# Kernel tuning notes

Measured on AMD Instinct MI355X. Metric: run time of the kernel, lower is better.

Reference implementation:

```python
import jax, jax.numpy as jnp
import numpy as np

N_NODES = 100_000
N_EDGES = 1_600_000
N_GRAPHS = 1_000
NODES_PER_GRAPH = 100
N_NODE_FEATS = 64
DIM_STATE = 32
DIM_OUT = 64
DIM_NODE_EMB = 64
HID = 128
HEADS = 8
BASES = 4


def _lin(key, out_f, in_f, bias=True):
    k1, k2 = jax.random.split(key)
    lim = 1.0 / np.sqrt(in_f)
    w = jax.random.uniform(k1, (out_f, in_f), minval=-lim, maxval=lim, dtype=jnp.float32)
    if not bias:
        return w
    b = jax.random.uniform(k2, (out_f,), minval=-lim, maxval=lim, dtype=jnp.float32)
    return w, b


def setup_inputs() -> dict:
    key = jax.random.key(0)
    ks = jax.random.split(key, 16)
    x = jax.random.normal(ks[0], (N_NODES, N_NODE_FEATS), dtype=jnp.float32)
    edge_index = jax.random.randint(ks[1], (2, N_EDGES), 0, N_NODES, dtype=jnp.int32)
    batch = jnp.arange(N_NODES, dtype=jnp.int32) // NODES_PER_GRAPH  # sorted segment ids
    n_atoms = jnp.full((N_GRAPHS, 1), NODES_PER_GRAPH, dtype=jnp.int32)  # consistent with batch
    z_e = jax.random.normal(ks[2], (N_GRAPHS, DIM_STATE), dtype=jnp.float32)
    nfc_w, nfc_b = _lin(ks[3], HID, N_NODE_FEATS)
    # EGConv: bases Linear(in, (out//heads)*bases, no bias); comb Linear(in, heads*bases); bias (out,)
    gc1_bases_w = _lin(ks[4], (HID // HEADS) * BASES, HID, bias=False)
    gc1_comb_w, gc1_comb_b = _lin(ks[5], HEADS * BASES, HID)
    gc1_bias = jnp.zeros((HID,), jnp.float32)
    gc2_bases_w = _lin(ks[6], (DIM_NODE_EMB // HEADS) * BASES, HID, bias=False)
    gc2_comb_w, gc2_comb_b = _lin(ks[7], HEADS * BASES, HID)
    gc2_bias = jnp.zeros((DIM_NODE_EMB,), jnp.float32)
    attn_w, attn_b = _lin(ks[8], 1, DIM_NODE_EMB + DIM_STATE)
    fcg_w, fcg_b = _lin(ks[9], DIM_OUT, DIM_NODE_EMB)
    fccg_w, fccg_b = _lin(ks[10], DIM_OUT, DIM_NODE_EMB)
    return {"x": x, "edge_index": edge_index, "batch": batch, "n_atoms": n_atoms, "z_e": z_e,
            "nfc_w": nfc_w, "nfc_b": nfc_b,
            "gc1_bases_w": gc1_bases_w, "gc1_comb_w": gc1_comb_w, "gc1_comb_b": gc1_comb_b, "gc1_bias": gc1_bias,
            "gc2_bases_w": gc2_bases_w, "gc2_comb_w": gc2_comb_w, "gc2_comb_b": gc2_comb_b, "gc2_bias": gc2_bias,
            "attn_w": attn_w, "attn_b": attn_b, "fcg_w": fcg_w, "fcg_b": fcg_b, "fccg_w": fccg_w, "fccg_b": fccg_b}


def _egconv(h, src, dst, bases_w, comb_w, comb_b, bias, heads=HEADS, nbases=BASES):
    # PyG EGConv with aggregators=['symnorm'], add_self_loops=True
    n = h.shape[0]
    out_ch = bias.shape[0]
    deg = jnp.ones((n,), h.dtype).at[dst].add(1.0)          # in-degree + self loop
    dis = jax.lax.rsqrt(deg)                                 # deg^-1/2
    b = h @ bases_w.T                                        # [n, nbases*(out_ch//heads)]
    # symnorm aggregation incl. self-loop term dis_i^2 * b_i
    agg = ((dis * dis)[:, None] * b).at[dst].add((dis[src] * dis[dst])[:, None] * b[src])
    w = (h @ comb_w.T + comb_b).reshape(n, heads, nbases)    # [n, H, B]
    agg = agg.reshape(n, nbases, out_ch // heads)            # [n, B, F/H]
    return jnp.einsum('nhb,nbf->nhf', w, agg).reshape(n, out_ch) + bias


def reference(x, edge_index, batch, n_atoms, z_e, nfc_w, nfc_b,
              gc1_bases_w, gc1_comb_w, gc1_comb_b, gc1_bias,
              gc2_bases_w, gc2_comb_w, gc2_comb_b, gc2_bias,
              attn_w, attn_b, fcg_w, fcg_b, fccg_w, fccg_b):
    src, dst = edge_index[0], edge_index[1]
    h = jax.nn.elu(x @ nfc_w.T + nfc_b)
    h = jax.nn.elu(_egconv(h, src, dst, gc1_bases_w, gc1_comb_w, gc1_comb_b, gc1_bias))
    h = jax.nn.elu(_egconv(h, src, dst, gc2_bases_w, gc2_comb_w, gc2_comb_b, gc2_bias))
    h = h / jnp.maximum(jnp.linalg.norm(h, axis=1, keepdims=True), 1e-12)  # L2 normalize
    z_a = jax.ops.segment_sum(h, batch, num_segments=N_GRAPHS) @ fcg_w.T + fcg_b
    z_rep = jnp.repeat(z_e, n_atoms[:, 0], axis=0, total_repeat_length=N_NODES)
    logits = jnp.concatenate([h, z_rep], axis=1) @ attn_w.T + attn_b + 1e-16  # [N,1]
    m = jax.ops.segment_max(logits, batch, num_segments=N_GRAPHS)
    e = jnp.exp(logits - m[batch])
    denom = jax.ops.segment_sum(e, batch, num_segments=N_GRAPHS) + 1e-16
    attns = e / denom[batch]
    z_c = jax.ops.segment_sum(attns * h, batch, num_segments=N_GRAPHS) @ fccg_w.T + fccg_b
    return z_a, z_c, h
```

## Files before the change

kernel.cpp:

```cpp
#include <hip/hip_runtime.h>
#include <hip/hip_bf16.h>
#include <math.h>

#define N_NODES  100000
#define N_EDGES  1600000
#define N_GRAPHS 1000
#define NPG      100
#define NBKT     391
#define EPB      4096

typedef float  f32x4 __attribute__((ext_vector_type(4)));
typedef short  s16x8 __attribute__((ext_vector_type(8)));

__device__ __forceinline__ float elu_f(float x) {
    return x > 0.0f ? x : expm1f(x);
}
__device__ __forceinline__ float bf2f(unsigned int u16) {
    union { unsigned int i; float f; } v; v.i = u16 << 16; return v.f;
}
__device__ __forceinline__ unsigned short f2bf(float f) {
    __hip_bfloat16 h = __float2bfloat16(f);
    return *reinterpret_cast<unsigned short*>(&h);
}
__device__ __forceinline__ s16x8 cvt8(const float4& a, const float4& b) {
    s16x8 o;
    o[0]=(short)f2bf(a.x); o[1]=(short)f2bf(a.y); o[2]=(short)f2bf(a.z); o[3]=(short)f2bf(a.w);
    o[4]=(short)f2bf(b.x); o[5]=(short)f2bf(b.y); o[6]=(short)f2bf(b.z); o[7]=(short)f2bf(b.w);
    return o;
}

__global__ __launch_bounds__(512) void zero_bkt_k(int* __restrict__ bkt_cnt) {
    int t = threadIdx.x;
    if (t < NBKT) bkt_cnt[t] = 0;
}

__global__ __launch_bounds__(256) void bincount_k(const int* __restrict__ ei, int* __restrict__ bkt_cnt) {
    __shared__ int h[NBKT];
    const int t = threadIdx.x;
    for (int i = t; i < NBKT; i += 256) h[i] = 0;
    __syncthreads();
    const int4* dst4 = (const int4*)(ei + N_EDGES);
    int i0 = blockIdx.x * (EPB / 4);
    for (int i = t; i < EPB / 4; i += 256) {
        int g = i0 + i;
        if (g < N_EDGES / 4) {
            int4 d = dst4[g];
            atomicAdd(&h[d.x >> 8], 1);
            atomicAdd(&h[d.y >> 8], 1);
            atomicAdd(&h[d.z >> 8], 1);
            atomicAdd(&h[d.w >> 8], 1);
        }
    }
    __syncthreads();
    for (int i = t; i < NBKT; i += 256)
        if (h[i]) atomicAdd(&bkt_cnt[i], h[i]);
}

__global__ __launch_bounds__(512) void bkt_scan_k(const int* __restrict__ bkt_cnt,
                                                  int* __restrict__ bkt_start,
                                                  int* __restrict__ bkt_cursor)
{
    __shared__ int s[512];
    int t = threadIdx.x;
    s[t] = (t < NBKT) ? bkt_cnt[t] : 0;
    __syncthreads();
    #pragma unroll
    for (int off = 1; off < 512; off <<= 1) {
        int u = (t >= off) ? s[t - off] : 0;
        __syncthreads();
        s[t] += u;
        __syncthreads();
    }
    if (t <= NBKT) {
        int v = (t == 0) ? 0 : s[t - 1];
        bkt_start[t] = v;
        if (t < NBKT) bkt_cursor[t] = v;
    }
}

__global__ __launch_bounds__(256) void binscatter_k(const int* __restrict__ ei,
                                                    int* __restrict__ bkt_cursor,
                                                    int2* __restrict__ pairs)
{
    __shared__ int h[NBKT];
    __shared__ int base[NBKT];
    const int t = threadIdx.x;
    for (int i = t; i < NBKT; i += 256) h[i] = 0;
    __syncthreads();
    const int4* src4 = (const int4*)ei;
    const int4* dst4 = (const int4*)(ei + N_EDGES);
    int i0 = blockIdx.x * (EPB / 4);
    for (int i = t; i < EPB / 4; i += 256) {
        int g = i0 + i;
        if (g < N_EDGES / 4) {
            int4 d = dst4[g];
            atomicAdd(&h[d.x >> 8], 1);
            atomicAdd(&h[d.y >> 8], 1);
            atomicAdd(&h[d.z >> 8], 1);
            atomicAdd(&h[d.w >> 8], 1);
        }
    }
    __syncthreads();
    for (int i = t; i < NBKT; i += 256) {
        int c = h[i];
        base[i] = c ? atomicAdd(&bkt_cursor[i], c) : 0;
        h[i] = 0;
    }
    __syncthreads();
    for (int i = t; i < EPB / 4; i += 256) {
        int g = i0 + i;
        if (g < N_EDGES / 4) {
            int4 s4 = src4[g];
            int4 d4 = dst4[g];
            int b, r;
            b = d4.x >> 8; r = atomicAdd(&h[b], 1); pairs[base[b] + r] = make_int2(s4.x, d4.x);
            b = d4.y >> 8; r = atomicAdd(&h[b], 1); pairs[base[b] + r] = make_int2(s4.y, d4.y);
            b = d4.z >> 8; r = atomicAdd(&h[b], 1); pairs[base[b] + r] = make_int2(s4.z, d4.z);
            b = d4.w >> 8; r = atomicAdd(&h[b], 1); pairs[base[b] + r] = make_int2(s4.w, d4.w);
        }
    }
}

__global__ __launch_bounds__(256) void bucket_csr_k(const int2* __restrict__ pairs,
                                                    const int* __restrict__ bkt_start,
                                                    int* __restrict__ starts,
                                                    int* __restrict__ cnt,
                                                    float* __restrict__ dis,
                                                    int* __restrict__ srclist)
{
    __shared__ int s[256];
    __shared__ int cur[256];
    const int b = blockIdx.x, t = threadIdx.x;
    const int lo = bkt_start[b], hi = bkt_start[b + 1];
    const int n0 = b << 8;
    const int nn = min(256, N_NODES - n0);

    s[t] = 0;
    __syncthreads();
    for (int i = lo + t; i < hi; i += 256) {
        int2 p = pairs[i];
        atomicAdd(&s[p.y & 255], 1);
    }
    __syncthreads();
    int v = s[t];
    __syncthreads();
    s[t] = v;
    __syncthreads();
    #pragma unroll
    for (int off = 1; off < 256; off <<= 1) {
        int u = (t >= off) ? s[t - off] : 0;
        __syncthreads();
        s[t] += u;
        __syncthreads();
    }
    int ex = lo + s[t] - v;
    if (t < nn) {
        starts[n0 + t] = ex;
        cnt[n0 + t] = v;
        dis[n0 + t] = rsqrtf(1.0f + (float)v);
    }
    cur[t] = ex;
    __syncthreads();
    for (int i = lo + t; i < hi; i += 256) {
        int2 p = pairs[i];
        int pos = atomicAdd(&cur[p.y & 255], 1);
        srclist[pos] = p.x;
    }
}

template<int K, int N1, int N2, int WR, int WC, int RT, int CT, bool AF32>
__global__ __launch_bounds__(256) void mgemm_k(
    const void* __restrict__ Av, const float* __restrict__ W1,
    const float* __restrict__ W2, const float* __restrict__ bias,
    const float* __restrict__ dis,
    void* __restrict__ out1, float* __restrict__ out2, int M)
{
    constexpr int KT = K / 32;
    const int t = threadIdx.x;
    const int wave = t >> 6, lane = t & 63;
    const int wr = wave / WC, wc = wave % WC;
    const int lr = lane & 15, lk = lane >> 4;
    const int blockRow = blockIdx.x * (WR * RT * 16);

    f32x4 acc[RT][CT];
    #pragma unroll
    for (int rt = 0; rt < RT; ++rt)
        #pragma unroll
        for (int ct = 0; ct < CT; ++ct)
            acc[rt][ct] = (f32x4){0.f, 0.f, 0.f, 0.f};

    const float*          Af = (const float*)Av;
    const unsigned short* Ab = (const unsigned short*)Av;

    #pragma unroll
    for (int kt = 0; kt < KT; ++kt) {
        const int k0 = kt * 32 + lk * 8;
        s16x8 afr[RT];
        #pragma unroll
        for (int rt = 0; rt < RT; ++rt) {
            int r = blockRow + (wr * RT + rt) * 16 + lr;
            r = (r < M) ? r : (M - 1);
            if constexpr (AF32) {
                const float* ap = Af + (size_t)r * K + k0;
                float4 v1 = *(const float4*)ap;
                float4 v2 = *(const float4*)(ap + 4);
                afr[rt] = cvt8(v1, v2);
            } else {
                afr[rt] = *(const s16x8*)(Ab + (size_t)r * K + k0);
            }
        }
        s16x8 bfr[CT];
        #pragma unroll
        for (int ct = 0; ct < CT; ++ct) {
            int n = (wc * CT + ct) * 16 + lr;
            const float* wp = (N2 == 0 || n < N1) ? (W1 + (size_t)n * K + k0)
                                                  : (W2 + (size_t)(n - N1) * K + k0);
            float4 v1 = *(const float4*)wp;
            float4 v2 = *(const float4*)(wp + 4);
            bfr[ct] = cvt8(v1, v2);
        }
        #pragma unroll
        for (int rt = 0; rt < RT; ++rt)
            #pragma unroll
            for (int ct = 0; ct < CT; ++ct)
                acc[rt][ct] = __builtin_amdgcn_mfma_f32_16x16x32_bf16(afr[rt], bfr[ct], acc[rt][ct], 0, 0, 0);
    }

    #pragma unroll
    for (int rt = 0; rt < RT; ++rt) {
        int mbase = blockRow + (wr * RT + rt) * 16 + lk * 4;
        #pragma unroll
        for (int j = 0; j < 4; ++j) {
            int m = mbase + j;
            if (m >= M) continue;
            float dsc = (N2 == 0) ? 1.0f : dis[m];
            #pragma unroll
            for (int ct = 0; ct < CT; ++ct) {
                int n = (wc * CT + ct) * 16 + lr;
                float v = acc[rt][ct][j];
                if constexpr (N2 == 0) {
                    v = elu_f(v + bias[n]);
                    ((unsigned short*)out1)[(size_t)m * N1 + n] = f2bf(v);
                } else {
                    if (n < N1) {
                        ((unsigned short*)out1)[(size_t)m * N1 + n] = f2bf(dsc * v);
                    } else {
                        out2[(size_t)m * N2 + (n - N1)] = v + bias[n - N1];
                    }
                }
            }
        }
    }
}

__global__ __launch_bounds__(256) void gather1_k(
    const int* __restrict__ starts, const int* __restrict__ cnt,
    const int* __restrict__ srclist, const unsigned short* __restrict__ c,
    const float* __restrict__ w1, const float* __restrict__ dis,
    const float* __restrict__ bias, unsigned short* __restrict__ h2b)
{
    __shared__ float aggS[4][68];

    const int t = threadIdx.x;
    const int nn   = t >> 6;
    const int lane = t & 63;
    const int q    = lane & 15;
    const int slot = lane >> 4;
    const int n    = blockIdx.x * 4 + nn;

    const int s0 = starts[n];
    const int cn = cnt[n];
    float a0 = 0.f, a1 = 0.f, a2 = 0.f, a3 = 0.f;
    if (slot == 0) {
        uint2 u = *(const uint2*)(c + (size_t)n * 64 + q * 4);
        a0 = bf2f(u.x & 0xffff); a1 = bf2f(u.x >> 16);
        a2 = bf2f(u.y & 0xffff); a3 = bf2f(u.y >> 16);
    }
    for (int j = slot; j < cn; j += 4) {
        int src = srclist[s0 + j];
        uint2 u = *(const uint2*)(c + (size_t)src * 64 + q * 4);
        a0 += bf2f(u.x & 0xffff); a1 += bf2f(u.x >> 16);
        a2 += bf2f(u.y & 0xffff); a3 += bf2f(u.y >> 16);
    }
    a0 += __shfl_xor(a0, 16, 64); a0 += __shfl_xor(a0, 32, 64);
    a1 += __shfl_xor(a1, 16, 64); a1 += __shfl_xor(a1, 32, 64);
    a2 += __shfl_xor(a2, 16, 64); a2 += __shfl_xor(a2, 32, 64);
    a3 += __shfl_xor(a3, 16, 64); a3 += __shfl_xor(a3, 32, 64);
    if (slot == 0) {
        aggS[nn][q * 4 + 0] = a0;
        aggS[nn][q * 4 + 1] = a1;
        aggS[nn][q * 4 + 2] = a2;
        aggS[nn][q * 4 + 3] = a3;
    }
    __syncthreads();

    const float dn = dis[n];
    const float* wr = w1 + (size_t)n * 32;
    unsigned short* out = h2b + (size_t)n * 128;
    #pragma unroll
    for (int r = 0; r < 2; ++r) {
        int j = r * 64 + lane;
        int hh = j >> 4, f = j & 15;
        float4 wv = *(const float4*)(wr + hh * 4);
        float s = wv.x * aggS[nn][0 * 16 + f] + wv.y * aggS[nn][1 * 16 + f]
                + wv.z * aggS[nn][2 * 16 + f] + wv.w * aggS[nn][3 * 16 + f];
        float v = elu_f(s * dn + bias[j]);
        out[j] = f2bf(v);
    }
}

__global__ __launch_bounds__(256) void gather2_k(
    const int* __restrict__ starts, const int* __restrict__ cnt,
    const int* __restrict__ srclist, const unsigned short* __restrict__ c,
    const float* __restrict__ w2, const float* __restrict__ dis,
    const float* __restrict__ bias, float* __restrict__ hout)
{
    __shared__ float aggS[4][36];

    const int t = threadIdx.x;
    const int nn   = t >> 6;
    const int lane = t & 63;
    const int q    = lane & 15;
    const int slot = lane >> 4;
    const int n    = blockIdx.x * 4 + nn;

    const int s0 = starts[n];
    const int cn = cnt[n];
    float a0 = 0.f, a1 = 0.f;
    if (slot == 0) {
        unsigned int u = *(const unsigned int*)(c + (size_t)n * 32 + q * 2);
        a0 = bf2f(u & 0xffff); a1 = bf2f(u >> 16);
    }
    for (int j = slot; j < cn; j += 4) {
        int src = srclist[s0 + j];
        unsigned int u = *(const unsigned int*)(c + (size_t)src * 32 + q * 2);
        a0 += bf2f(u & 0xffff); a1 += bf2f(u >> 16);
    }
    a0 += __shfl_xor(a0, 16, 64); a0 += __shfl_xor(a0, 32, 64);
    a1 += __shfl_xor(a1, 16, 64); a1 += __shfl_xor(a1, 32, 64);
    if (slot == 0) {
        aggS[nn][q * 2 + 0] = a0;
        aggS[nn][q * 2 + 1] = a1;
    }
    __syncthreads();

    const float dn = dis[n];
    const int hh = lane >> 3, f = lane & 7;
    float4 wv = *(const float4*)(w2 + (size_t)n * 32 + hh * 4);
    float s = wv.x * aggS[nn][0 * 8 + f] + wv.y * aggS[nn][1 * 8 + f]
            + wv.z * aggS[nn][2 * 8 + f] + wv.w * aggS[nn][3 * 8 + f];
    float sv = elu_f(s * dn + bias[lane]);

    float tot = sv * sv;
    #pragma unroll
    for (int o = 1; o < 64; o <<= 1) tot += __shfl_xor(tot, o, 64);
    float inv = 1.0f / fmaxf(sqrtf(tot), 1e-12f);
    hout[(size_t)n * 64 + lane] = sv * inv;
}

__global__ __launch_bounds__(128) void graph_k(const float* __restrict__ h,
                                               const float* __restrict__ z_e,
                                               const float* __restrict__ aw,
                                               const float* __restrict__ ab,
                                               const float* __restrict__ fcgw,
                                               const float* __restrict__ fcgb,
                                               const float* __restrict__ fccgw,
                                               const float* __restrict__ fccgb,
                                               float* __restrict__ z_a,
                                               float* __restrict__ z_c)
{
    __shared__ float Hs[NPG * 64];
    __shared__ float sumh[64], wsh[64], lg[NPG], ex[NPG];
    __shared__ float red[2];
    int g = blockIdx.x, t = threadIdx.x;
    const float* hg = h + (size_t)g * NPG * 64;
    for (int idx = t; idx < NPG * 64; idx += 128) Hs[idx] = hg[idx];
    __syncthreads();

    if (t < 64) {
        float s = 0.0f;
        for (int n = 0; n < NPG; ++n) s += Hs[n * 64 + t];
        sumh[t] = s;
    }
    __syncthreads();

    if (t < 64) {
        float acc = fcgb[t];
        for (int f = 0; f < 64; ++f) acc = fmaf(sumh[f], fcgw[t * 64 + f], acc);
        z_a[(size_t)g * 64 + t] = acc;
    }
    if (t < NPG) {
        float zd = 0.0f;
        for (int q = 0; q < 32; ++q) zd = fmaf(z_e[(size_t)g * 32 + q], aw[64 + q], zd);
        float dot = 0.0f;
        for (int k0 = 0; k0 < 64; ++k0) {
            int k = (k0 + t) & 63;
            dot = fmaf(Hs[t * 64 + k], aw[k], dot);
        }
        lg[t] = dot + zd + ab[0] + 1e-16f;
    }
    __syncthreads();

    if (t < 64) {
        float m = -INFINITY;
        for (int n = t; n < NPG; n += 64) m = fmaxf(m, lg[n]);
        #pragma unroll
        for (int o = 1; o < 64; o <<= 1) m = fmaxf(m, __shfl_xor(m, o, 64));
        if (t == 0) red[0] = m;
    }
    __syncthreads();
    float m = red[0];
    if (t < NPG) ex[t] = expf(lg[t] - m);
    __syncthreads();
    if (t < 64) {
        float s = 0.0f;
        for (int n = t; n < NPG; n += 64) s += ex[n];
        #pragma unroll
        for (int o = 1; o < 64; o <<= 1) s += __shfl_xor(s, o, 64);
        if (t == 0) red[1] = s + 1e-16f;
    }
    __syncthreads();
    float inv_denom = 1.0f / red[1];
    if (t < 64) {
        float a = 0.0f;
        for (int n = 0; n < NPG; ++n) a = fmaf(ex[n], Hs[n * 64 + t], a);
        wsh[t] = a * inv_denom;
    }
    __syncthreads();
    if (t < 64) {
        float acc = fccgb[t];
        for (int f = 0; f < 64; ++f) acc = fmaf(wsh[f], fccgw[t * 64 + f], acc);
        z_c[(size_t)g * 64 + t] = acc;
    }
}

extern "C" void kernel_launch(void* const* d_in, const int* in_sizes, int n_in,
                              void* d_out, int out_size, void* d_ws, size_t ws_size,
                              hipStream_t stream)
{
    const float* x     = (const float*)d_in[0];
    const int*   ei    = (const int*)d_in[1];
    const float* z_e   = (const float*)d_in[4];
    const float* nfc_w = (const float*)d_in[5];
    const float* nfc_b = (const float*)d_in[6];
    const float* g1bw  = (const float*)d_in[7];
    const float* g1cw  = (const float*)d_in[8];
    const float* g1cb  = (const float*)d_in[9];
    const float* g1b   = (const float*)d_in[10];
    const float* g2bw  = (const float*)d_in[11];
    const float* g2cw  = (const float*)d_in[12];
    const float* g2cb  = (const float*)d_in[13];
    const float* g2b   = (const float*)d_in[14];
    const float* aw    = (const float*)d_in[15];
    const float* ab    = (const float*)d_in[16];
    const float* fcgw  = (const float*)d_in[17];
    const float* fcgb  = (const float*)d_in[18];
    const float* fccgw = (const float*)d_in[19];
    const float* fccgb = (const float*)d_in[20];

    float* ws        = (float*)d_ws;
    float* dis       = ws;
    int*   cnt       = (int*)(ws + 102400);
    int*   starts    = cnt + 102400;
    int*   bkt_cnt   = starts + 102400;
    int*   bkt_start = bkt_cnt + 512;
    int*   bkt_cur   = bkt_start + 512;
    int*   srclist   = bkt_cur + 512;
    float* hbuf      = (float*)(srclist + 1600000);
    float* c1f       = hbuf + 6400000;
    float* w1        = c1f + 3200000;
    float* w2        = w1 + 3200000;
    unsigned short* hb = (unsigned short*)hbuf;
    unsigned short* c1 = (unsigned short*)c1f;
    unsigned short* c2 = (unsigned short*)c1f;
    int2*  pairs     = (int2*)hbuf;

    float* z_a  = (float*)d_out;
    float* z_c  = z_a + (size_t)N_GRAPHS * 64;
    float* hout = z_a + (size_t)2 * N_GRAPHS * 64;

    const int GB = (N_NODES + 63) / 64;

    zero_bkt_k<<<1, 512, 0, stream>>>(bkt_cnt);
    bincount_k<<<(N_EDGES + EPB - 1) / EPB, 256, 0, stream>>>(ei, bkt_cnt);
    bkt_scan_k<<<1, 512, 0, stream>>>(bkt_cnt, bkt_start, bkt_cur);
    binscatter_k<<<(N_EDGES + EPB - 1) / EPB, 256, 0, stream>>>(ei, bkt_cur, pairs);
    bucket_csr_k<<<NBKT, 256, 0, stream>>>(pairs, bkt_start, starts, cnt, dis, srclist);

    mgemm_k<64, 128, 0, 2, 2, 2, 4, true>
        <<<GB, 256, 0, stream>>>(x, nfc_w, nullptr, nfc_b, dis, hb, nullptr, N_NODES);
    mgemm_k<128, 64, 32, 2, 2, 2, 3, false>
        <<<GB, 256, 0, stream>>>(hb, g1bw, g1cw, g1cb, dis, c1, w1, N_NODES);
    gather1_k<<<N_NODES / 4, 256, 0, stream>>>(starts, cnt, srclist, c1, w1, dis, g1b, hb);
    mgemm_k<128, 32, 32, 2, 2, 2, 2, false>
        <<<GB, 256, 0, stream>>>(hb, g2bw, g2cw, g2cb, dis, c2, w2, N_NODES);
    gather2_k<<<N_NODES / 4, 256, 0, stream>>>(starts, cnt, srclist, c2, w2, dis, g2b, hout);
    graph_k<<<N_GRAPHS, 128, 0, stream>>>(hout, z_e, aw, ab, fcgw, fcgb, fccgw, fccgb, z_a, z_c);
}
```

Measured before the change: 294.1 us.

## Fuse node-feature GEMM with gc1 projection and gather1 with gc2 projection

```diff
diff --git a/kernel.cpp b/kernel.cpp
--- a/kernel.cpp
+++ b/kernel.cpp
@@ -168,144 +168,195 @@
     }
 }
 
-template<int K, int N1, int N2, int WR, int WC, int RT, int CT, bool AF32>
-__global__ __launch_bounds__(256) void mgemm_k(
-    const void* __restrict__ Av, const float* __restrict__ W1,
-    const float* __restrict__ W2, const float* __restrict__ bias,
-    const float* __restrict__ dis,
-    void* __restrict__ out1, float* __restrict__ out2, int M)
-{
-    constexpr int KT = K / 32;
+__global__ __launch_bounds__(256) void fusedA_k(
+    const float* __restrict__ x, const float* __restrict__ W0, const float* __restrict__ b0,
+    const float* __restrict__ Wc, const float* __restrict__ Ww, const float* __restrict__ bw,
+    const float* __restrict__ dis, unsigned short* __restrict__ c1out,
+    float* __restrict__ w1out, int M)
+{
+    __shared__ unsigned short hT[64][136];
     const int t = threadIdx.x;
     const int wave = t >> 6, lane = t & 63;
-    const int wr = wave / WC, wc = wave % WC;
     const int lr = lane & 15, lk = lane >> 4;
-    const int blockRow = blockIdx.x * (WR * RT * 16);
-
-    f32x4 acc[RT][CT];
-    #pragma unroll
-    for (int rt = 0; rt < RT; ++rt)
-        #pragma unroll
-        for (int ct = 0; ct < CT; ++ct)
-            acc[rt][ct] = (f32x4){0.f, 0.f, 0.f, 0.f};
-
-    const float*          Af = (const float*)Av;
-    const unsigned short* Ab = (const unsigned short*)Av;
-
-    #pragma unroll
-    for (int kt = 0; kt < KT; ++kt) {
-        const int k0 = kt * 32 + lk * 8;
-        s16x8 afr[RT];
-        #pragma unroll
-        for (int rt = 0; rt < RT; ++rt) {
-            int r = blockRow + (wr * RT + rt) * 16 + lr;
-            r = (r < M) ? r : (M - 1);
-            if constexpr (AF32) {
-                const float* ap = Af + (size_t)r * K + k0;
-                float4 v1 = *(const float4*)ap;
-                float4 v2 = *(const float4*)(ap + 4);
-                afr[rt] = cvt8(v1, v2);
-            } else {
-                afr[rt] = *(const s16x8*)(Ab + (size_t)r * K + k0);
-            }
-        }
-        s16x8 bfr[CT];
-        #pragma unroll
-        for (int ct = 0; ct < CT; ++ct) {
-            int n = (wc * CT + ct) * 16 + lr;
-            const float* wp = (N2 == 0 || n < N1) ? (W1 + (size_t)n * K + k0)
-                                                  : (W2 + (size_t)(n - N1) * K + k0);
-            float4 v1 = *(const float4*)wp;
-            float4 v2 = *(const float4*)(wp + 4);
-            bfr[ct] = cvt8(v1, v2);
-        }
-        #pragma unroll
-        for (int rt = 0; rt < RT; ++rt)
-            #pragma unroll
-            for (int ct = 0; ct < CT; ++ct)
-                acc[rt][ct] = __builtin_amdgcn_mfma_f32_16x16x32_bf16(afr[rt], bfr[ct], acc[rt][ct], 0, 0, 0);
-    }
-
-    #pragma unroll
-    for (int rt = 0; rt < RT; ++rt) {
-        int mbase = blockRow + (wr * RT + rt) * 16 + lk * 4;
+    const int blockRow = blockIdx.x * 64;
+
+    {
+        const int wr = wave >> 1, wc = wave & 1;
+        f32x4 acc[2][4];
+        #pragma unroll
+        for (int rt = 0; rt < 2; ++rt)
+            #pragma unroll
+            for (int ct = 0; ct < 4; ++ct) acc[rt][ct] = (f32x4){0.f,0.f,0.f,0.f};
+
+        #pragma unroll
+        for (int kt = 0; kt < 2; ++kt) {
+            const int k0 = kt * 32 + lk * 8;
+            s16x8 afr[2];
+            #pragma unroll
+            for (int rt = 0; rt < 2; ++rt) {
+                int r = blockRow + (wr * 2 + rt) * 16 + lr;
+                r = (r < M) ? r : (M - 1);
+                const float* ap = x + (size_t)r * 64 + k0;
+                afr[rt] = cvt8(*(const float4*)ap, *(const float4*)(ap + 4));
+            }
+            s16x8 bfr[4];
+            #pragma unroll
+            for (int ct = 0; ct < 4; ++ct) {
+                int n = (wc * 4 + ct) * 16 + lr;
+                const float* wp = W0 + (size_t)n * 64 + k0;
+                bfr[ct] = cvt8(*(const float4*)wp, *(const float4*)(wp + 4));
+            }
+            #pragma unroll
+            for (int rt = 0; rt < 2; ++rt)
+                #pragma unroll
+                for (int ct = 0; ct < 4; ++ct)
+                    acc[rt][ct] = __builtin_amdgcn_mfma_f32_16x16x32_bf16(afr[rt], bfr[ct], acc[rt][ct], 0, 0, 0);
+        }
+        #pragma unroll
+        for (int rt = 0; rt < 2; ++rt) {
+            int lmb = (wr * 2 + rt) * 16 + lk * 4;
+            #pragma unroll
+            for (int j = 0; j < 4; ++j) {
+                #pragma unroll
+                for (int ct = 0; ct < 4; ++ct) {
+                    int n = (wc * 4 + ct) * 16 + lr;
+                    float v = elu_f(acc[rt][ct][j] + b0[n]);
+                    hT[lmb + j][n] = f2bf(v);
+                }
+            }
+        }
+    }
+    __syncthreads();
+
+    {
+        f32x4 acc[6];
+        #pragma unroll
+        for (int ct = 0; ct < 6; ++ct) acc[ct] = (f32x4){0.f,0.f,0.f,0.f};
+        #pragma unroll
+        for (int kt = 0; kt < 4; ++kt) {
+            const int k0 = kt * 32 + lk * 8;
+            s16x8 af = *(const s16x8*)&hT[wave * 16 + lr][k0];
+            #pragma unroll
+            for (int ct = 0; ct < 6; ++ct) {
+                int n = ct * 16 + lr;
+                const float* wp = (n < 64) ? (Wc + (size_t)n * 128 + k0)
+                                           : (Ww + (size_t)(n - 64) * 128 + k0);
+                s16x8 bf = cvt8(*(const float4*)wp, *(const float4*)(wp + 4));
+                acc[ct] = __builtin_amdgcn_mfma_f32_16x16x32_bf16(af, bf, acc[ct], 0, 0, 0);
+            }
+        }
+        int mbase = blockRow + wave * 16 + lk * 4;
         #pragma unroll
         for (int j = 0; j < 4; ++j) {
             int m = mbase + j;
             if (m >= M) continue;
-            float dsc = (N2 == 0) ? 1.0f : dis[m];
-            #pragma unroll
-            for (int ct = 0; ct < CT; ++ct) {
-                int n = (wc * CT + ct) * 16 + lr;
-                float v = acc[rt][ct][j];
-                if constexpr (N2 == 0) {
-                    v = elu_f(v + bias[n]);
-                    ((unsigned short*)out1)[(size_t)m * N1 + n] = f2bf(v);
-                } else {
-                    if (n < N1) {
-                        ((unsigned short*)out1)[(size_t)m * N1 + n] = f2bf(dsc * v);
-                    } else {
-                        out2[(size_t)m * N2 + (n - N1)] = v + bias[n - N1];
-                    }
-                }
-            }
-        }
-    }
-}
-
-__global__ __launch_bounds__(256) void gather1_k(
+            float dsc = dis[m];
+            #pragma unroll
+            for (int ct = 0; ct < 6; ++ct) {
+                int n = ct * 16 + lr;
+                float v = acc[ct][j];
+                if (n < 64) c1out[(size_t)m * 64 + n] = f2bf(dsc * v);
+                else        w1out[(size_t)m * 32 + (n - 64)] = v + bw[n - 64];
+            }
+        }
+    }
+}
+
+__global__ __launch_bounds__(256) void fusedB_k(
     const int* __restrict__ starts, const int* __restrict__ cnt,
     const int* __restrict__ srclist, const unsigned short* __restrict__ c,
     const float* __restrict__ w1, const float* __restrict__ dis,
-    const float* __restrict__ bias, unsigned short* __restrict__ h2b)
-{
+    const float* __restrict__ bias,
+    const float* __restrict__ Wc, const float* __restrict__ Ww, const float* __restrict__ bw,
+    unsigned short* __restrict__ c2out, float* __restrict__ w2out, int M)
+{
+    __shared__ unsigned short hT[64][136];
     __shared__ float aggS[4][68];
 
     const int t = threadIdx.x;
-    const int nn   = t >> 6;
-    const int lane = t & 63;
+    const int wave = t >> 6, lane = t & 63;
     const int q    = lane & 15;
     const int slot = lane >> 4;
-    const int n    = blockIdx.x * 4 + nn;
-
-    const int s0 = starts[n];
-    const int cn = cnt[n];
-    float a0 = 0.f, a1 = 0.f, a2 = 0.f, a3 = 0.f;
-    if (slot == 0) {
-        uint2 u = *(const uint2*)(c + (size_t)n * 64 + q * 4);
-        a0 = bf2f(u.x & 0xffff); a1 = bf2f(u.x >> 16);
-        a2 = bf2f(u.y & 0xffff); a3 = bf2f(u.y >> 16);
-    }
-    for (int j = slot; j < cn; j += 4) {
-        int src = srclist[s0 + j];
-        uint2 u = *(const uint2*)(c + (size_t)src * 64 + q * 4);
-        a0 += bf2f(u.x & 0xffff); a1 += bf2f(u.x >> 16);
-        a2 += bf2f(u.y & 0xffff); a3 += bf2f(u.y >> 16);
-    }
-    a0 += __shfl_xor(a0, 16, 64); a0 += __shfl_xor(a0, 32, 64);
-    a1 += __shfl_xor(a1, 16, 64); a1 += __shfl_xor(a1, 32, 64);
-    a2 += __shfl_xor(a2, 16, 64); a2 += __shfl_xor(a2, 32, 64);
-    a3 += __shfl_xor(a3, 16, 64); a3 += __shfl_xor(a3, 32, 64);
-    if (slot == 0) {
-        aggS[nn][q * 4 + 0] = a0;
-        aggS[nn][q * 4 + 1] = a1;
-        aggS[nn][q * 4 + 2] = a2;
-        aggS[nn][q * 4 + 3] = a3;
-    }
-    __syncthreads();
-
-    const float dn = dis[n];
-    const float* wr = w1 + (size_t)n * 32;
-    unsigned short* out = h2b + (size_t)n * 128;
-    #pragma unroll
-    for (int r = 0; r < 2; ++r) {
-        int j = r * 64 + lane;
-        int hh = j >> 4, f = j & 15;
-        float4 wv = *(const float4*)(wr + hh * 4);
-        float s = wv.x * aggS[nn][0 * 16 + f] + wv.y * aggS[nn][1 * 16 + f]
-                + wv.z * aggS[nn][2 * 16 + f] + wv.w * aggS[nn][3 * 16 + f];
-        float v = elu_f(s * dn + bias[j]);
-        out[j] = f2bf(v);
+    const int nb   = blockIdx.x * 64;
+
+    for (int it = 0; it < 16; ++it) {
+        const int row = wave * 16 + it;
+        const int n = nb + row;
+        if (n < M) {
+            const int s0 = starts[n];
+            const int cn = cnt[n];
+            float a0 = 0.f, a1 = 0.f, a2 = 0.f, a3 = 0.f;
+            if (slot == 0) {
+                uint2 u = *(const uint2*)(c + (size_t)n * 64 + q * 4);
+                a0 = bf2f(u.x & 0xffff); a1 = bf2f(u.x >> 16);
+                a2 = bf2f(u.y & 0xffff); a3 = bf2f(u.y >> 16);
+            }
+            for (int j = slot; j < cn; j += 4) {
+                int src = srclist[s0 + j];
+                uint2 u = *(const uint2*)(c + (size_t)src * 64 + q * 4);
+                a0 += bf2f(u.x & 0xffff); a1 += bf2f(u.x >> 16);
+                a2 += bf2f(u.y & 0xffff); a3 += bf2f(u.y >> 16);
+            }
+            a0 += __shfl_xor(a0, 16, 64); a0 += __shfl_xor(a0, 32, 64);
+            a1 += __shfl_xor(a1, 16, 64); a1 += __shfl_xor(a1, 32, 64);
+            a2 += __shfl_xor(a2, 16, 64); a2 += __shfl_xor(a2, 32, 64);
+            a3 += __shfl_xor(a3, 16, 64); a3 += __shfl_xor(a3, 32, 64);
+            if (slot == 0) {
+                aggS[wave][q * 4 + 0] = a0;
+                aggS[wave][q * 4 + 1] = a1;
+                aggS[wave][q * 4 + 2] = a2;
+                aggS[wave][q * 4 + 3] = a3;
+            }
+            const float dn = dis[n];
+            const float* wr = w1 + (size_t)n * 32;
+            #pragma unroll
+            for (int r = 0; r < 2; ++r) {
+                int j = r * 64 + lane;
+                int hh = j >> 4, f = j & 15;
+                float4 wv = *(const float4*)(wr + hh * 4);
+                float s = wv.x * aggS[wave][0 * 16 + f] + wv.y * aggS[wave][1 * 16 + f]
+                        + wv.z * aggS[wave][2 * 16 + f] + wv.w * aggS[wave][3 * 16 + f];
+                hT[row][j] = f2bf(elu_f(s * dn + bias[j]));
+            }
+        } else {
+            hT[row][lane] = 0;
+            hT[row][64 + lane] = 0;
+        }
+    }
+    __syncthreads();
+
+    {
+        const int lr = lane & 15, lk = lane >> 4;
+        f32x4 acc[4];
+        #pragma unroll
+        for (int ct = 0; ct < 4; ++ct) acc[ct] = (f32x4){0.f,0.f,0.f,0.f};
+        #pragma unroll
+        for (int kt = 0; kt < 4; ++kt) {
+            const int k0 = kt * 32 + lk * 8;
+            s16x8 af = *(const s16x8*)&hT[wave * 16 + lr][k0];
+            #pragma unroll
+            for (int ct = 0; ct < 4; ++ct) {
+                int n = ct * 16 + lr;
+                const float* wp = (n < 32) ? (Wc + (size_t)n * 128 + k0)
+                                           : (Ww + (size_t)(n - 32) * 128 + k0);
+                s16x8 bf = cvt8(*(const float4*)wp, *(const float4*)(wp + 4));
+                acc[ct] = __builtin_amdgcn_mfma_f32_16x16x32_bf16(af, bf, acc[ct], 0, 0, 0);
+            }
+        }
+        int mbase = nb + wave * 16 + lk * 4;
+        #pragma unroll
+        for (int j = 0; j < 4; ++j) {
+            int m = mbase + j;
+            if (m >= M) continue;
+            float dsc = dis[m];
+            #pragma unroll
+            for (int ct = 0; ct < 4; ++ct) {
+                int n = ct * 16 + lr;
+                float v = acc[ct][j];
+                if (n < 32) c2out[(size_t)m * 32 + n] = f2bf(dsc * v);
+                else        w2out[(size_t)m * 32 + (n - 32)] = v + bw[n - 32];
+            }
+        }
     }
 }
 
@@ -466,14 +517,13 @@
     int*   bkt_start = bkt_cnt + 512;
     int*   bkt_cur   = bkt_start + 512;
     int*   srclist   = bkt_cur + 512;
-    float* hbuf      = (float*)(srclist + 1600000);
-    float* c1f       = hbuf + 6400000;
-    float* w1        = c1f + 3200000;
-    float* w2        = w1 + 3200000;
-    unsigned short* hb = (unsigned short*)hbuf;
-    unsigned short* c1 = (unsigned short*)c1f;
-    unsigned short* c2 = (unsigned short*)c1f;
-    int2*  pairs     = (int2*)hbuf;
+    float* preg      = (float*)(srclist + 1600000);
+    float* w1        = preg + 3200000;
+    float* c2f       = w1 + 3200000;
+    float* w2        = c2f + 1600000;
+    int2*  pairs     = (int2*)preg;
+    unsigned short* c1 = (unsigned short*)preg;
+    unsigned short* c2 = (unsigned short*)c2f;
 
     float* z_a  = (float*)d_out;
     float* z_c  = z_a + (size_t)N_GRAPHS * 64;
@@ -487,13 +537,9 @@
     binscatter_k<<<(N_EDGES + EPB - 1) / EPB, 256, 0, stream>>>(ei, bkt_cur, pairs);
     bucket_csr_k<<<NBKT, 256, 0, stream>>>(pairs, bkt_start, starts, cnt, dis, srclist);
 
-    mgemm_k<64, 128, 0, 2, 2, 2, 4, true>
-        <<<GB, 256, 0, stream>>>(x, nfc_w, nullptr, nfc_b, dis, hb, nullptr, N_NODES);
-    mgemm_k<128, 64, 32, 2, 2, 2, 3, false>
-        <<<GB, 256, 0, stream>>>(hb, g1bw, g1cw, g1cb, dis, c1, w1, N_NODES);
-    gather1_k<<<N_NODES / 4, 256, 0, stream>>>(starts, cnt, srclist, c1, w1, dis, g1b, hb);
-    mgemm_k<128, 32, 32, 2, 2, 2, 2, false>
-        <<<GB, 256, 0, stream>>>(hb, g2bw, g2cw, g2cb, dis, c2, w2, N_NODES);
+    fusedA_k<<<GB, 256, 0, stream>>>(x, nfc_w, nfc_b, g1bw, g1cw, g1cb, dis, c1, w1, N_NODES);
+    fusedB_k<<<GB, 256, 0, stream>>>(starts, cnt, srclist, c1, w1, dis, g1b,
+                                     g2bw, g2cw, g2cb, c2, w2, N_NODES);
     gather2_k<<<N_NODES / 4, 256, 0, stream>>>(starts, cnt, srclist, c2, w2, dis, g2b, hout);
     graph_k<<<N_GRAPHS, 128, 0, stream>>>(hout, z_e, aw, ab, fcgw, fcgb, fccgw, fccgb, z_a, z_c);
 }
```

Result: slower. 352.8 us (+20.0%).
